# Optimization experiments

Hardware: AMD Instinct MI355X
Metric: run time of the kernel (lower is better)

## Reference

```python
import jax, jax.numpy as jnp
import numpy as np

B = 512      # batch
T = 16       # tokens per instruction
V = 1000     # vocab
E = 4        # num_experts
K = 1        # active experts per layer
NLAYERS = 3
TOPK_LOGIC = 32


def _conv(x, w, b, stride=2):
    # x: [B,Cin,H,W], w: [Cout,Cin,3,3] (OIHW), padding=1, stride=2
    y = jax.lax.conv_general_dilated(
        x, w, window_strides=(stride, stride), padding=((1, 1), (1, 1)),
        dimension_numbers=('NCHW', 'OIHW', 'NCHW'))
    return y + b[None, :, None, None]


def _gated_conv(x, w, b, gate):
    # w: [E,Cout,Cin,3,3], b: [E,Cout], gate: [B,E] 0/1 mask
    # Faithful to original: all experts computed densely, then masked.
    outs = jax.vmap(lambda wi, bi: _conv(x, wi, bi))(w, b)  # [E,B,Cout,H',W']
    return jnp.einsum('ebchw,be->bchw', outs, gate)


def _topk_mask(logits, k):
    # 0/1 mask with ones at the top-k positions along the last axis
    _, idx = jax.lax.top_k(logits, k)
    return jnp.sum(jax.nn.one_hot(idx, logits.shape[-1], dtype=logits.dtype), axis=-2)


def setup_inputs() -> dict:
    key = jax.random.key(0)
    ks = jax.random.split(key, 16)
    def rn(k, shape, s=0.05):
        return jax.random.normal(k, shape, jnp.float32) * s
    return dict(
        img=jax.random.normal(ks[0], (B, 12, 56, 56), jnp.float32),
        text=jax.random.randint(ks[1], (B, T), 0, V),
        prev_action=jax.random.randint(ks[2], (B,), 0, 7),
        emb_table=rn(ks[3], (V, 32), 1.0),
        r_w1=rn(ks[4], (32, 64)), r_b1=jnp.zeros((64,), jnp.float32),
        r_w2=rn(ks[5], (64, NLAYERS * E)), r_b2=jnp.zeros((NLAYERS * E,), jnp.float32),
        l_w1=rn(ks[6], (32, 64)), l_b1=jnp.zeros((64,), jnp.float32),
        l_w2=rn(ks[7], (64, 256)), l_b2=jnp.zeros((256,), jnp.float32),
        c1_w=rn(ks[8], (E, 32, 12, 3, 3)), c1_b=jnp.zeros((E, 32), jnp.float32),
        c2_w=rn(ks[9], (E, 64, 32, 3, 3)), c2_b=jnp.zeros((E, 64), jnp.float32),
        c3_w=rn(ks[10], (E, 128, 64, 3, 3)), c3_b=jnp.zeros((E, 128), jnp.float32),
        act_emb=rn(ks[11], (7, 16), 1.0),
        f_w=rn(ks[12], (6272 + 32 + 16, 256)), f_b=jnp.zeros((256,), jnp.float32),
        h_w=rn(ks[13], (256, 5)), h_b=jnp.zeros((5,), jnp.float32),
    )


def reference(img, text, prev_action, emb_table, r_w1, r_b1, r_w2, r_b2,
              l_w1, l_b1, l_w2, l_b2, c1_w, c1_b, c2_w, c2_b, c3_w, c3_b,
              act_emb, f_w, f_b, h_w, h_b):
    # EmbeddingBag(mode='mean') over token dim
    lang = jnp.mean(emb_table[text], axis=1)                      # [B,32]
    # Router: MLP -> [B,3,E] logits, top-k scatter -> 0/1 mask
    rlog = (jax.nn.relu(lang @ r_w1 + r_b1) @ r_w2 + r_b2).reshape(-1, NLAYERS, E)
    masks = _topk_mask(rlog, K)                                   # [B,3,E]
    x = jax.nn.relu(_gated_conv(img, c1_w, c1_b, masks[:, 0, :])) # [B,32,28,28]
    x = jax.nn.relu(_gated_conv(x, c2_w, c2_b, masks[:, 1, :]))   # [B,64,14,14]
    x = jax.nn.relu(_gated_conv(x, c3_w, c3_b, masks[:, 2, :]))   # [B,128,7,7]
    vis = x.reshape(x.shape[0], -1)                               # [B,6272]
    act = act_emb[prev_action]                                    # [B,16]
    fused = jnp.concatenate([vis, lang, act], axis=1)             # [B,6320]
    hidden = fused @ f_w + f_b                                    # [B,256]
    logic = jax.nn.relu(lang @ l_w1 + l_b1) @ l_w2 + l_b2         # [B,256]
    lmask = _topk_mask(logic, TOPK_LOGIC)                         # [B,256]
    out = jax.nn.relu(hidden * lmask)                             # dropout is identity in eval
    logits = out @ h_w + h_b                                      # [B,5]
    return logits, rlog
```

## Files before the change

### kernel.cpp

```cpp
#include <hip/hip_runtime.h>
#include <hip/hip_bf16.h>


typedef __bf16 bf16x8 __attribute__((ext_vector_type(8)));
typedef float f32x4 __attribute__((ext_vector_type(4)));

__device__ __forceinline__ unsigned short f2bf(float f) {
  union { float f; unsigned u; } v; v.f = f;
  unsigned r = v.u + 0x7FFFu + ((v.u >> 16) & 1u);
  return (unsigned short)(r >> 16);
}

__global__ __launch_bounds__(256) void router_kernel(
    const int* __restrict__ text, const float* __restrict__ emb,
    const float* __restrict__ r_w1, const float* __restrict__ r_b1,
    const float* __restrict__ r_w2, const float* __restrict__ r_b2,
    const float* __restrict__ l_w1, const float* __restrict__ l_b1,
    const float* __restrict__ l_w2, const float* __restrict__ l_b2,
    const float* __restrict__ act_emb, const int* __restrict__ pa,
    float* __restrict__ rlog_out, int* __restrict__ eidx, float* __restrict__ lmask,
    unsigned short* __restrict__ tailb) {
  int b = blockIdx.x;
  int t = threadIdx.x;
  __shared__ float lg[32];
  __shared__ float hr[64];
  __shared__ float hl[64];
  __shared__ float rl[12];
  __shared__ float lgc[256];

  if (t < 32) {
    const int* tb = text + b * 16;
    float s = 0.f;
#pragma unroll
    for (int tok = 0; tok < 16; ++tok) s += emb[tb[tok] * 32 + t];
    lg[t] = s * 0.0625f;
  }
  __syncthreads();

  if (t < 64) {
    float s1 = r_b1[t], s2 = l_b1[t];
    for (int k = 0; k < 32; ++k) {
      float lv = lg[k];
      s1 += lv * r_w1[k * 64 + t];
      s2 += lv * l_w1[k * 64 + t];
    }
    hr[t] = fmaxf(s1, 0.f);
    hl[t] = fmaxf(s2, 0.f);
  }
  if (t < 64) {
    float v = 0.f;
    if (t < 32) v = lg[t];
    else if (t < 48) v = act_emb[pa[b] * 16 + (t - 32)];
    tailb[b * 64 + t] = f2bf(v);
  }
  __syncthreads();

  if (t < 12) {
    float s = r_b2[t];
    for (int k = 0; k < 64; ++k) s += hr[k] * r_w2[k * 12 + t];
    rl[t] = s;
    rlog_out[b * 12 + t] = s;
  }
  {
    float s = l_b2[t];
    for (int k = 0; k < 64; ++k) s += hl[k] * l_w2[k * 256 + t];
    lgc[t] = s;
  }
  __syncthreads();

  if (t < 3) {
    int best = 0;
    float bv = rl[t * 4];
    for (int e = 1; e < 4; ++e) {
      float v = rl[t * 4 + e];
      if (v > bv) { bv = v; best = e; }
    }
    eidx[b * 3 + t] = best;
  }
  {
    float v = lgc[t];
    int cnt = 0;
    for (int k = 0; k < 256; ++k) {
      float u = lgc[k];
      cnt += (u > v) || (u == v && k < t);
    }
    lmask[b * 256 + t] = (cnt < 32) ? 1.f : 0.f;
  }
}

__global__ __launch_bounds__(256) void prep_kernel(
    const float* __restrict__ img,
    const float* __restrict__ c1_w, const float* __restrict__ c2_w,
    const float* __restrict__ c3_w, const float* __restrict__ fw,
    const int* __restrict__ eidx,
    unsigned short* __restrict__ x0b,
    unsigned short* __restrict__ wb1, unsigned short* __restrict__ wb2,
    unsigned short* __restrict__ wb3, unsigned short* __restrict__ fwT,
    int* __restrict__ cnt, int* __restrict__ perm) {
  __shared__ __align__(16) char shm[64 * 72 * 2];
  const int blk = blockIdx.x;
  const int tid = threadIdx.x;

  if (blk < 6272) {
    int idx = blk * 256 + tid;
    int s = idx / 3136;
    int p = idx - s * 3136;
    const float* ib = img + (size_t)s * 37632 + p;
    unsigned short v[16];
#pragma unroll
    for (int ci = 0; ci < 12; ++ci) v[ci] = f2bf(ib[ci * 3136]);
#pragma unroll
    for (int ci = 12; ci < 16; ++ci) v[ci] = 0;
    uint4* dst = (uint4*)(x0b + (size_t)idx * 16);
    dst[0] = *(const uint4*)&v[0];
    dst[1] = *(const uint4*)&v[8];
  } else if (blk < 7840) {
    int idx = (blk - 6272) * 256 + tid;
    if (idx < 24576) {
      int k = idx % 192, ec = idx / 192;
      float v = 0.f;
      if (k < 144) {
        int g = k >> 4, ci = k & 15;
        if (ci < 12) v = c1_w[ec * 108 + ci * 9 + g];
      }
      wb1[idx] = f2bf(v);
    } else if (idx < 106496) {
      int i2 = idx - 24576;
      int k = i2 % 320, ec = i2 / 320;
      float v = 0.f;
      if (k < 288) {
        int g = k >> 5, ci = k & 31;
        v = c2_w[ec * 288 + ci * 9 + g];
      }
      wb2[i2] = f2bf(v);
    } else {
      int i3 = idx - 106496;
      int k = i3 % 576, ec = i3 / 576;
      int g = k >> 6, ci = k & 63;
      wb3[i3] = f2bf(c3_w[ec * 576 + ci * 9 + g]);
    }
  } else if (blk < 8236) {
    unsigned short(*tl)[72] = (unsigned short(*)[72])shm;
    int fb = blk - 7840;
    int kblk = fb >> 2, nblk = fb & 3;
    int n0 = nblk * 64;
    int k0 = kblk * 64;
    int rl = tid >> 2;
    int c4 = (tid & 3) * 16;
    int srow;
    bool valid;
    if (kblk < 98) {
      int p = kblk >> 1;
      int c0 = (kblk & 1) * 64;
      srow = (c0 + rl) * 49 + p;
      valid = true;
    } else {
      srow = 6272 + rl;
      valid = (rl < 48);
    }
#pragma unroll
    for (int h = 0; h < 4; ++h) {
      float4 v = valid ? *(const float4*)&fw[(size_t)srow * 256 + n0 + c4 + h * 4]
                       : (float4){0.f, 0.f, 0.f, 0.f};
      tl[rl][c4 + h * 4 + 0] = f2bf(v.x);
      tl[rl][c4 + h * 4 + 1] = f2bf(v.y);
      tl[rl][c4 + h * 4 + 2] = f2bf(v.z);
      tl[rl][c4 + h * 4 + 3] = f2bf(v.w);
    }
    __syncthreads();
    int nloc = tid >> 2;
    int kc = (tid & 3) * 16;
    unsigned short vv[16];
#pragma unroll
    for (int i = 0; i < 16; ++i) vv[i] = tl[kc + i][nloc];
    unsigned short* dst = fwT + (size_t)(n0 + nloc) * 6336 + k0 + kc;
    *(uint4*)dst = *(const uint4*)&vv[0];
    *(uint4*)(dst + 8) = *(const uint4*)&vv[8];
  } else {
    int* el = (int*)shm;
    int* cc = el + 512;
    int l = blk - 8236;
    el[tid] = eidx[tid * 3 + l];
    el[tid + 256] = eidx[(tid + 256) * 3 + l];
    __syncthreads();
    if (tid < 4) {
      int c = 0;
      for (int b = 0; b < 512; ++b) c += (el[b] == tid);
      cc[tid] = c;
      cnt[l * 4 + tid] = c;
    }
    __syncthreads();
#pragma unroll
    for (int rep = 0; rep < 2; ++rep) {
      int b = tid + rep * 256;
      int e = el[b];
      int rank = 0;
      for (int bp = 0; bp < b; ++bp) rank += (el[bp] == e);
      int off = 0;
      for (int ee = 0; ee < e; ++ee) off += cc[ee];
      perm[l * 512 + off + rank] = b;
    }
  }
}

template<int CIN, int H, int OH, int KREAL, int KP, int COUT,
         int WGM, int WGN, int MF, int NF>
__global__ __launch_bounds__(256) void conv_mfma(
    const unsigned short* __restrict__ in, const unsigned short* __restrict__ wb,
    const float* __restrict__ bias, const int* __restrict__ cnt,
    const int* __restrict__ perm, unsigned short* __restrict__ out) {
  constexpr int PerS = OH * OH;
  constexpr int BM = WGM * MF * 16;
  constexpr int BN = WGN * NF * 16;
  constexpr int AJ = BM / 32;
  constexpr int KT = KP / 64;
  constexpr int W = H;
  constexpr int BCH = BN / 32;

  int bm = blockIdx.x;
  int e = 0, row0 = 0, rows = 0;
  bool found = false;
  {
    int acc = 0, ebase = 0;
#pragma unroll
    for (int ee = 0; ee < 4; ++ee) {
      int er = cnt[ee] * PerS;
      int te = (er + BM - 1) / BM;
      if (!found && bm < acc + te) {
        e = ee;
        row0 = ebase + (bm - acc) * BM;
        rows = er - (bm - acc) * BM;
        if (rows > BM) rows = BM;
        found = true;
      }
      acc += te;
      ebase += er;
    }
  }
  if (!found) return;

  __shared__ __align__(16) char lds[BM * 128 + BN * 128];
  char* ldsB = lds + BM * 128;
  const int tid = threadIdx.x;
  const int lane = tid & 63;
  const int wid = tid >> 6;
  const int wm0 = (wid / WGN) * (MF * 16);
  const int wn0 = (wid % WGN) * (NF * 16);
  const int c16 = tid & 7;

  int ihc[AJ], iwc[AJ], abase[AJ], adso[AJ];
#pragma unroll
  for (int j = 0; j < AJ; ++j) {
    int r = (tid >> 3) + 32 * j;
    int gr = row0 + r;
    const int MAXR = 512 * PerS - 1;
    if (gr > MAXR) gr = MAXR;
    int sord = gr / PerS;
    int p = gr - sord * PerS;
    int s = perm[sord];
    int oh = p / OH, ow = p - oh * OH;
    ihc[j] = oh * 2 - 1;
    iwc[j] = ow * 2 - 1;
    abase[j] = s * (H * W);
    adso[j] = r * 128 + ((c16 * 16) ^ ((r & 7) << 4));
  }
  const unsigned short* wbe = wb + (size_t)e * COUT * KP;
  int bgo[BCH], bdso[BCH];
#pragma unroll
  for (int c = 0; c < BCH; ++c) {
    int cc = tid + 256 * c;
    int n = cc >> 3, cb = cc & 7;
    bgo[c] = n * KP + cb * 8;
    bdso[c] = n * 128 + ((cb * 16) ^ ((n & 7) << 4));
  }
  int ardo[MF], arx[MF], brdo[NF], brx[NF];
#pragma unroll
  for (int mf = 0; mf < MF; ++mf) {
    int r = wm0 + mf * 16 + (lane & 15);
    ardo[mf] = r * 128;
    arx[mf] = (r & 7) << 4;
  }
#pragma unroll
  for (int nf = 0; nf < NF; ++nf) {
    int n = wn0 + nf * 16 + (lane & 15);
    brdo[nf] = n * 128;
    brx[nf] = (n & 7) << 4;
  }

  auto loadA = [&](int kt, int j) -> uint4 {
    uint4 z; z.x = z.y = z.z = z.w = 0u;
    int kbase = kt * 64 + c16 * 8;
    if (kbase >= KREAL) return z;
    int g = kbase / CIN;
    int ci0 = kbase - g * CIN;
    int kh = g / 3, kw = g - (g / 3) * 3;
    int ih = ihc[j] + kh, iw = iwc[j] + kw;
    if ((unsigned)ih >= (unsigned)H || (unsigned)iw >= (unsigned)W) return z;
    const unsigned short* p = in + ((size_t)(abase[j] + ih * W + iw) * CIN + ci0);
    return *(const uint4*)p;
  };

  uint4 rA[AJ], rB[BCH];
#pragma unroll
  for (int j = 0; j < AJ; ++j) rA[j] = loadA(0, j);
#pragma unroll
  for (int c = 0; c < BCH; ++c) rB[c] = *(const uint4*)(wbe + bgo[c]);

  f32x4 acc[MF][NF];
#pragma unroll
  for (int mf = 0; mf < MF; ++mf)
#pragma unroll
    for (int nf = 0; nf < NF; ++nf) acc[mf][nf] = (f32x4){0.f, 0.f, 0.f, 0.f};

  for (int kt = 0; kt < KT; ++kt) {
    __syncthreads();
#pragma unroll
    for (int j = 0; j < AJ; ++j) *(uint4*)(lds + adso[j]) = rA[j];
#pragma unroll
    for (int c = 0; c < BCH; ++c) *(uint4*)(ldsB + bdso[c]) = rB[c];
    __syncthreads();
    if (kt + 1 < KT) {
#pragma unroll
      for (int j = 0; j < AJ; ++j) rA[j] = loadA(kt + 1, j);
#pragma unroll
      for (int c = 0; c < BCH; ++c) rB[c] = *(const uint4*)(wbe + bgo[c] + (kt + 1) * 64);
    }
#pragma unroll
    for (int ks = 0; ks < 2; ++ks) {
      int cb = ks * 64 + ((lane >> 4) << 4);
      bf16x8 af[MF], bfv[NF];
#pragma unroll
      for (int mf = 0; mf < MF; ++mf)
        af[mf] = __builtin_bit_cast(bf16x8, *(const uint4*)(lds + ardo[mf] + (cb ^ arx[mf])));
#pragma unroll
      for (int nf = 0; nf < NF; ++nf)
        bfv[nf] = __builtin_bit_cast(bf16x8, *(const uint4*)(ldsB + brdo[nf] + (cb ^ brx[nf])));
#pragma unroll
      for (int mf = 0; mf < MF; ++mf)
#pragma unroll
        for (int nf = 0; nf < NF; ++nf)
          acc[mf][nf] = __builtin_amdgcn_mfma_f32_16x16x32_bf16(af[mf], bfv[nf], acc[mf][nf], 0, 0, 0);
    }
  }

  const int col = lane & 15;
  const int rg = (lane >> 4) * 4;
#pragma unroll
  for (int mf = 0; mf < MF; ++mf) {
#pragma unroll
    for (int r = 0; r < 4; ++r) {
      int m = wm0 + mf * 16 + rg + r;
      if (m < rows) {
        int gr = row0 + m;
        int sord = gr / PerS;
        int p = gr - sord * PerS;
        int s = perm[sord];
        size_t ob = ((size_t)s * PerS + p) * COUT;
#pragma unroll
        for (int nf = 0; nf < NF; ++nf) {
          int co = wn0 + nf * 16 + col;
          float v = acc[mf][nf][r] + bias[e * COUT + co];
          out[ob + co] = f2bf(fmaxf(v, 0.f));
        }
      }
    }
  }
}

__global__ __launch_bounds__(256) void fgemm_kernel(
    const unsigned short* __restrict__ x3, const unsigned short* __restrict__ tail,
    const unsigned short* __restrict__ fwT, float* __restrict__ partial) {
  constexpr int MF = 2, NF = 2;
  const int row0 = blockIdx.x * 64;
  const int nc0 = blockIdx.y * 64;
  const int kz = blockIdx.z * 704;
  __shared__ __align__(16) char lds[64 * 128 + 64 * 128];
  char* ldsB = lds + 64 * 128;
  const int tid = threadIdx.x;
  const int lane = tid & 63;
  const int wid = tid >> 6;
  const int wm0 = (wid >> 1) * 32;
  const int wn0 = (wid & 1) * 32;
  const int c16 = tid & 7;
  int arow[2], adso[2];
#pragma unroll
  for (int j = 0; j < 2; ++j) {
    int r = (tid >> 3) + 32 * j;
    arow[j] = row0 + r;
    adso[j] = r * 128 + ((c16 * 16) ^ ((r & 7) << 4));
  }
  int bgo[2], bdso[2];
#pragma unroll
  for (int c = 0; c < 2; ++c) {
    int cc = tid + 256 * c;
    int n = cc >> 3, cb = cc & 7;
    bgo[c] = (nc0 + n) * 6336 + kz + cb * 8;
    bdso[c] = n * 128 + ((cb * 16) ^ ((n & 7) << 4));
  }
  int ardo[MF], arx[MF], brdo[NF], brx[NF];
#pragma unroll
  for (int mf = 0; mf < MF; ++mf) {
    int r = wm0 + mf * 16 + (lane & 15);
    ardo[mf] = r * 128; arx[mf] = (r & 7) << 4;
  }
#pragma unroll
  for (int nf = 0; nf < NF; ++nf) {
    int n = wn0 + nf * 16 + (lane & 15);
    brdo[nf] = n * 128; brx[nf] = (n & 7) << 4;
  }
  auto loadA = [&](int kt, int j) -> uint4 {
    int k = kz + kt * 64 + c16 * 8;
    const unsigned short* p;
    if (k < 6272) p = x3 + (size_t)arow[j] * 6272 + k;
    else p = tail + arow[j] * 64 + (k - 6272);
    return *(const uint4*)p;
  };
  uint4 rA[2], rB[2];
#pragma unroll
  for (int j = 0; j < 2; ++j) rA[j] = loadA(0, j);
#pragma unroll
  for (int c = 0; c < 2; ++c) rB[c] = *(const uint4*)(fwT + bgo[c]);
  f32x4 acc[MF][NF];
#pragma unroll
  for (int mf = 0; mf < MF; ++mf)
#pragma unroll
    for (int nf = 0; nf < NF; ++nf) acc[mf][nf] = (f32x4){0.f, 0.f, 0.f, 0.f};

  for (int kt = 0; kt < 11; ++kt) {
    __syncthreads();
#pragma unroll
    for (int j = 0; j < 2; ++j) *(uint4*)(lds + adso[j]) = rA[j];
#pragma unroll
    for (int c = 0; c < 2; ++c) *(uint4*)(ldsB + bdso[c]) = rB[c];
    __syncthreads();
    if (kt + 1 < 11) {
#pragma unroll
      for (int j = 0; j < 2; ++j) rA[j] = loadA(kt + 1, j);
#pragma unroll
      for (int c = 0; c < 2; ++c) rB[c] = *(const uint4*)(fwT + bgo[c] + (kt + 1) * 64);
    }
#pragma unroll
    for (int ks = 0; ks < 2; ++ks) {
      int cb = ks * 64 + ((lane >> 4) << 4);
      bf16x8 af[MF], bfv[NF];
#pragma unroll
      for (int mf = 0; mf < MF; ++mf)
        af[mf] = __builtin_bit_cast(bf16x8, *(const uint4*)(lds + ardo[mf] + (cb ^ arx[mf])));
#pragma unroll
      for (int nf = 0; nf < NF; ++nf)
        bfv[nf] = __builtin_bit_cast(bf16x8, *(const uint4*)(ldsB + brdo[nf] + (cb ^ brx[nf])));
#pragma unroll
      for (int mf = 0; mf < MF; ++mf)
#pragma unroll
        for (int nf = 0; nf < NF; ++nf)
          acc[mf][nf] = __builtin_amdgcn_mfma_f32_16x16x32_bf16(af[mf], bfv[nf], acc[mf][nf], 0, 0, 0);
    }
  }
  const int col = lane & 15;
  const int rg = (lane >> 4) * 4;
  float* pz = partial + (size_t)blockIdx.z * 131072;
#pragma unroll
  for (int mf = 0; mf < MF; ++mf)
#pragma unroll
    for (int r = 0; r < 4; ++r) {
      int m = wm0 + mf * 16 + rg + r;
      int grow = row0 + m;
#pragma unroll
      for (int nf = 0; nf < NF; ++nf) {
        int n = nc0 + wn0 + nf * 16 + col;
        pz[grow * 256 + n] = acc[mf][nf][r];
      }
    }
}

__global__ __launch_bounds__(256) void reduce_head(const float* __restrict__ part,
                                                   const float* __restrict__ f_b,
                                                   const float* __restrict__ lmask,
                                                   const float* __restrict__ h_w,
                                                   const float* __restrict__ h_b,
                                                   float* __restrict__ logits) {
  int b = blockIdx.x, t = threadIdx.x;
  float s = f_b[t];
#pragma unroll
  for (int z = 0; z < 9; ++z) s += part[z * 131072 + b * 256 + t];
  __shared__ float o[256];
  o[t] = (lmask[b * 256 + t] != 0.f) ? fmaxf(s, 0.f) : 0.f;
  __syncthreads();
  if (t < 5) {
    float v = h_b[t];
    for (int n = 0; n < 256; ++n) v += o[n] * h_w[n * 5 + t];
    logits[b * 5 + t] = v;
  }
}

extern "C" void kernel_launch(void* const* d_in, const int* in_sizes, int n_in,
                              void* d_out, int out_size, void* d_ws, size_t ws_size,
                              hipStream_t stream) {
  (void)in_sizes; (void)n_in; (void)out_size; (void)ws_size;
  const float* img       = (const float*)d_in[0];
  const int*   text      = (const int*)d_in[1];
  const int*   pa        = (const int*)d_in[2];
  const float* emb_table = (const float*)d_in[3];
  const float* r_w1 = (const float*)d_in[4];
  const float* r_b1 = (const float*)d_in[5];
  const float* r_w2 = (const float*)d_in[6];
  const float* r_b2 = (const float*)d_in[7];
  const float* l_w1 = (const float*)d_in[8];
  const float* l_b1 = (const float*)d_in[9];
  const float* l_w2 = (const float*)d_in[10];
  const float* l_b2 = (const float*)d_in[11];
  const float* c1_w = (const float*)d_in[12];
  const float* c1_b = (const float*)d_in[13];
  const float* c2_w = (const float*)d_in[14];
  const float* c2_b = (const float*)d_in[15];
  const float* c3_w = (const float*)d_in[16];
  const float* c3_b = (const float*)d_in[17];
  const float* act_emb = (const float*)d_in[18];
  const float* f_w = (const float*)d_in[19];
  const float* f_b = (const float*)d_in[20];
  const float* h_w = (const float*)d_in[21];
  const float* h_b = (const float*)d_in[22];

  float* outf   = (float*)d_out;
  float* logits = outf;
  float* rlog   = outf + 2560;

  char* cur = (char*)d_ws;
  auto alloc = [&](size_t bytes) { char* r = cur; cur += (bytes + 255) & ~(size_t)255; return r; };
  float* lmask   = (float*)alloc(131072 * 4);
  int* eidx      = (int*)alloc(1536 * 4);
  int* cnt       = (int*)alloc(12 * 4);
  int* perm      = (int*)alloc(1536 * 4);
  unsigned short* wb1  = (unsigned short*)alloc((size_t)24576 * 2);
  unsigned short* wb2  = (unsigned short*)alloc((size_t)81920 * 2);
  unsigned short* wb3  = (unsigned short*)alloc((size_t)294912 * 2);
  unsigned short* fwT  = (unsigned short*)alloc((size_t)1622016 * 2);
  unsigned short* tailb= (unsigned short*)alloc((size_t)32768 * 2);
  unsigned short* x1b  = (unsigned short*)alloc((size_t)12845056 * 2);
  unsigned short* x0b  = (unsigned short*)alloc((size_t)25690112 * 2);
  unsigned short* x2b  = x0b;
  unsigned short* x3b  = x0b + 6422528;
  float* partial       = (float*)(x0b + 6422528 + 3211264);

  router_kernel<<<512, 256, 0, stream>>>(text, emb_table, r_w1, r_b1, r_w2, r_b2,
                                         l_w1, l_b1, l_w2, l_b2, act_emb, pa,
                                         rlog, eidx, lmask, tailb);
  prep_kernel<<<8239, 256, 0, stream>>>(img, c1_w, c2_w, c3_w, f_w, eidx,
                                        x0b, wb1, wb2, wb3, fwT, cnt, perm);

  conv_mfma<16, 56, 28, 144, 192, 32, 4, 1, 2, 2>
      <<<3139, 256, 0, stream>>>(x0b, wb1, c1_b, cnt + 0, perm + 0, x1b);
  conv_mfma<32, 28, 14, 288, 320, 64, 2, 2, 4, 2>
      <<<787, 256, 0, stream>>>(x1b, wb2, c2_b, cnt + 4, perm + 512, x2b);
  conv_mfma<64, 14, 7, 576, 576, 128, 1, 4, 4, 2>
      <<<395, 256, 0, stream>>>(x2b, wb3, c3_b, cnt + 8, perm + 1024, x3b);

  fgemm_kernel<<<dim3(8, 4, 9), 256, 0, stream>>>(x3b, tailb, fwT, partial);
  reduce_head<<<512, 256, 0, stream>>>(partial, f_b, lmask, h_w, h_b, logits);
}
```

Baseline: 160.2 us.

## Fuse router into prep kernel, split bucketing out, vectorize image conversion

The router work moves into the prep kernel as its first 512 blocks, so it runs alongside the weight and image conversion. The expert bucketing, which needs the router output, moves into its own small kernel launched after prep. This keeps the launch count the same but lets router work overlap with prep. The image NCHW→NHWC bf16 conversion now handles 4 pixels per thread with float4 loads, which cuts the prep grid from 8239 to 4044 blocks at the cost of more registers per thread.

```diff
diff --git a/kernel.cpp b/kernel.cpp
--- a/kernel.cpp
+++ b/kernel.cpp
@@ -11,111 +11,94 @@
   return (unsigned short)(r >> 16);
 }
 
-__global__ __launch_bounds__(256) void router_kernel(
+__global__ __launch_bounds__(256) void prep_kernel(
+    const float* __restrict__ img,
     const int* __restrict__ text, const float* __restrict__ emb,
     const float* __restrict__ r_w1, const float* __restrict__ r_b1,
     const float* __restrict__ r_w2, const float* __restrict__ r_b2,
     const float* __restrict__ l_w1, const float* __restrict__ l_b1,
     const float* __restrict__ l_w2, const float* __restrict__ l_b2,
     const float* __restrict__ act_emb, const int* __restrict__ pa,
-    float* __restrict__ rlog_out, int* __restrict__ eidx, float* __restrict__ lmask,
-    unsigned short* __restrict__ tailb) {
-  int b = blockIdx.x;
-  int t = threadIdx.x;
-  __shared__ float lg[32];
-  __shared__ float hr[64];
-  __shared__ float hl[64];
-  __shared__ float rl[12];
-  __shared__ float lgc[256];
-
-  if (t < 32) {
-    const int* tb = text + b * 16;
-    float s = 0.f;
-#pragma unroll
-    for (int tok = 0; tok < 16; ++tok) s += emb[tb[tok] * 32 + t];
-    lg[t] = s * 0.0625f;
-  }
-  __syncthreads();
-
-  if (t < 64) {
-    float s1 = r_b1[t], s2 = l_b1[t];
-    for (int k = 0; k < 32; ++k) {
-      float lv = lg[k];
-      s1 += lv * r_w1[k * 64 + t];
-      s2 += lv * l_w1[k * 64 + t];
-    }
-    hr[t] = fmaxf(s1, 0.f);
-    hl[t] = fmaxf(s2, 0.f);
-  }
-  if (t < 64) {
-    float v = 0.f;
-    if (t < 32) v = lg[t];
-    else if (t < 48) v = act_emb[pa[b] * 16 + (t - 32)];
-    tailb[b * 64 + t] = f2bf(v);
-  }
-  __syncthreads();
-
-  if (t < 12) {
-    float s = r_b2[t];
-    for (int k = 0; k < 64; ++k) s += hr[k] * r_w2[k * 12 + t];
-    rl[t] = s;
-    rlog_out[b * 12 + t] = s;
-  }
-  {
-    float s = l_b2[t];
-    for (int k = 0; k < 64; ++k) s += hl[k] * l_w2[k * 256 + t];
-    lgc[t] = s;
-  }
-  __syncthreads();
-
-  if (t < 3) {
-    int best = 0;
-    float bv = rl[t * 4];
-    for (int e = 1; e < 4; ++e) {
-      float v = rl[t * 4 + e];
-      if (v > bv) { bv = v; best = e; }
-    }
-    eidx[b * 3 + t] = best;
-  }
-  {
-    float v = lgc[t];
-    int cnt = 0;
-    for (int k = 0; k < 256; ++k) {
-      float u = lgc[k];
-      cnt += (u > v) || (u == v && k < t);
-    }
-    lmask[b * 256 + t] = (cnt < 32) ? 1.f : 0.f;
-  }
-}
-
-__global__ __launch_bounds__(256) void prep_kernel(
-    const float* __restrict__ img,
     const float* __restrict__ c1_w, const float* __restrict__ c2_w,
     const float* __restrict__ c3_w, const float* __restrict__ fw,
-    const int* __restrict__ eidx,
+    float* __restrict__ rlog_out, int* __restrict__ eidx, float* __restrict__ lmask,
+    unsigned short* __restrict__ tailb,
     unsigned short* __restrict__ x0b,
     unsigned short* __restrict__ wb1, unsigned short* __restrict__ wb2,
-    unsigned short* __restrict__ wb3, unsigned short* __restrict__ fwT,
-    int* __restrict__ cnt, int* __restrict__ perm) {
+    unsigned short* __restrict__ wb3, unsigned short* __restrict__ fwT) {
   __shared__ __align__(16) char shm[64 * 72 * 2];
   const int blk = blockIdx.x;
   const int tid = threadIdx.x;
 
-  if (blk < 6272) {
-    int idx = blk * 256 + tid;
-    int s = idx / 3136;
-    int p = idx - s * 3136;
-    const float* ib = img + (size_t)s * 37632 + p;
-    unsigned short v[16];
-#pragma unroll
-    for (int ci = 0; ci < 12; ++ci) v[ci] = f2bf(ib[ci * 3136]);
-#pragma unroll
-    for (int ci = 12; ci < 16; ++ci) v[ci] = 0;
-    uint4* dst = (uint4*)(x0b + (size_t)idx * 16);
-    dst[0] = *(const uint4*)&v[0];
-    dst[1] = *(const uint4*)&v[8];
-  } else if (blk < 7840) {
-    int idx = (blk - 6272) * 256 + tid;
+  if (blk < 512) {
+    int b = blk;
+    int t = tid;
+    __shared__ float lg[32];
+    __shared__ float hr[64];
+    __shared__ float hl[64];
+    __shared__ float rl[12];
+    __shared__ float lgc[256];
+
+    if (t < 32) {
+      const int* tb = text + b * 16;
+      float s = 0.f;
+#pragma unroll
+      for (int tok = 0; tok < 16; ++tok) s += emb[tb[tok] * 32 + t];
+      lg[t] = s * 0.0625f;
+    }
+    __syncthreads();
+
+    if (t < 64) {
+      float s1 = r_b1[t], s2 = l_b1[t];
+      for (int k = 0; k < 32; ++k) {
+        float lv = lg[k];
+        s1 += lv * r_w1[k * 64 + t];
+        s2 += lv * l_w1[k * 64 + t];
+      }
+      hr[t] = fmaxf(s1, 0.f);
+      hl[t] = fmaxf(s2, 0.f);
+    }
+    if (t < 64) {
+      float v = 0.f;
+      if (t < 32) v = lg[t];
+      else if (t < 48) v = act_emb[pa[b] * 16 + (t - 32)];
+      tailb[b * 64 + t] = f2bf(v);
+    }
+    __syncthreads();
+
+    if (t < 12) {
+      float s = r_b2[t];
+      for (int k = 0; k < 64; ++k) s += hr[k] * r_w2[k * 12 + t];
+      rl[t] = s;
+      rlog_out[b * 12 + t] = s;
+    }
+    {
+      float s = l_b2[t];
+      for (int k = 0; k < 64; ++k) s += hl[k] * l_w2[k * 256 + t];
+      lgc[t] = s;
+    }
+    __syncthreads();
+
+    if (t < 3) {
+      int best = 0;
+      float bv = rl[t * 4];
+      for (int e = 1; e < 4; ++e) {
+        float v = rl[t * 4 + e];
+        if (v > bv) { bv = v; best = e; }
+      }
+      eidx[b * 3 + t] = best;
+    }
+    {
+      float v = lgc[t];
+      int cnt = 0;
+      for (int k = 0; k < 256; ++k) {
+        float u = lgc[k];
+        cnt += (u > v) || (u == v && k < t);
+      }
+      lmask[b * 256 + t] = (cnt < 32) ? 1.f : 0.f;
+    }
+  } else if (blk < 2080) {
+    int idx = (blk - 512) * 256 + tid;
     if (idx < 24576) {
       int k = idx % 192, ec = idx / 192;
       float v = 0.f;
@@ -139,9 +122,9 @@
       int g = k >> 6, ci = k & 63;
       wb3[i3] = f2bf(c3_w[ec * 576 + ci * 9 + g]);
     }
-  } else if (blk < 8236) {
+  } else if (blk < 2476) {
     unsigned short(*tl)[72] = (unsigned short(*)[72])shm;
-    int fb = blk - 7840;
+    int fb = blk - 2080;
     int kblk = fb >> 2, nblk = fb & 3;
     int n0 = nblk * 64;
     int k0 = kblk * 64;
@@ -177,29 +160,57 @@
     *(uint4*)dst = *(const uint4*)&vv[0];
     *(uint4*)(dst + 8) = *(const uint4*)&vv[8];
   } else {
-    int* el = (int*)shm;
-    int* cc = el + 512;
-    int l = blk - 8236;
-    el[tid] = eidx[tid * 3 + l];
-    el[tid + 256] = eidx[(tid + 256) * 3 + l];
-    __syncthreads();
-    if (tid < 4) {
-      int c = 0;
-      for (int b = 0; b < 512; ++b) c += (el[b] == tid);
-      cc[tid] = c;
-      cnt[l * 4 + tid] = c;
-    }
-    __syncthreads();
-#pragma unroll
-    for (int rep = 0; rep < 2; ++rep) {
-      int b = tid + rep * 256;
-      int e = el[b];
-      int rank = 0;
-      for (int bp = 0; bp < b; ++bp) rank += (el[bp] == e);
-      int off = 0;
-      for (int ee = 0; ee < e; ++ee) off += cc[ee];
-      perm[l * 512 + off + rank] = b;
-    }
+    int idx4 = (blk - 2476) * 256 + tid;
+    int s = idx4 / 784;
+    int q = idx4 - s * 784;
+    const float* ib = img + (size_t)s * 37632 + q * 4;
+    float4 v[12];
+#pragma unroll
+    for (int ci = 0; ci < 12; ++ci) v[ci] = *(const float4*)&ib[ci * 3136];
+    unsigned short o16[64];
+#pragma unroll
+    for (int j = 0; j < 4; ++j) {
+      o16[j * 16 + 0]  = f2bf(j == 0 ? v[0].x : j == 1 ? v[0].y : j == 2 ? v[0].z : v[0].w);
+#pragma unroll
+      for (int ci = 1; ci < 12; ++ci) {
+        float fv = (j == 0) ? v[ci].x : (j == 1) ? v[ci].y : (j == 2) ? v[ci].z : v[ci].w;
+        o16[j * 16 + ci] = f2bf(fv);
+      }
+#pragma unroll
+      for (int ci = 12; ci < 16; ++ci) o16[j * 16 + ci] = 0;
+    }
+    uint4* dst = (uint4*)(x0b + (size_t)idx4 * 64);
+#pragma unroll
+    for (int h = 0; h < 8; ++h) dst[h] = *(const uint4*)&o16[h * 8];
+  }
+}
+
+__global__ __launch_bounds__(256) void bucket_kernel(const int* __restrict__ eidx,
+                                                     int* __restrict__ cnt,
+                                                     int* __restrict__ perm) {
+  int l = blockIdx.x;
+  __shared__ int el[512];
+  __shared__ int cc[4];
+  int t = threadIdx.x;
+  el[t] = eidx[t * 3 + l];
+  el[t + 256] = eidx[(t + 256) * 3 + l];
+  __syncthreads();
+  if (t < 4) {
+    int c = 0;
+    for (int b = 0; b < 512; ++b) c += (el[b] == t);
+    cc[t] = c;
+    cnt[l * 4 + t] = c;
+  }
+  __syncthreads();
+#pragma unroll
+  for (int rep = 0; rep < 2; ++rep) {
+    int b = t + rep * 256;
+    int e = el[b];
+    int rank = 0;
+    for (int bp = 0; bp < b; ++bp) rank += (el[bp] == e);
+    int off = 0;
+    for (int ee = 0; ee < e; ++ee) off += cc[ee];
+    perm[l * 512 + off + rank] = b;
   }
 }
 
@@ -542,11 +553,14 @@
   unsigned short* x3b  = x0b + 6422528;
   float* partial       = (float*)(x0b + 6422528 + 3211264);
 
-  router_kernel<<<512, 256, 0, stream>>>(text, emb_table, r_w1, r_b1, r_w2, r_b2,
-                                         l_w1, l_b1, l_w2, l_b2, act_emb, pa,
-                                         rlog, eidx, lmask, tailb);
-  prep_kernel<<<8239, 256, 0, stream>>>(img, c1_w, c2_w, c3_w, f_w, eidx,
-                                        x0b, wb1, wb2, wb3, fwT, cnt, perm);
+  prep_kernel<<<4044, 256, 0, stream>>>(img, text, emb_table,
+                                        r_w1, r_b1, r_w2, r_b2,
+                                        l_w1, l_b1, l_w2, l_b2,
+                                        act_emb, pa,
+                                        c1_w, c2_w, c3_w, f_w,
+                                        rlog, eidx, lmask, tailb,
+                                        x0b, wb1, wb2, wb3, fwT);
+  bucket_kernel<<<3, 256, 0, stream>>>(eidx, cnt, perm);
 
   conv_mfma<16, 56, 28, 144, 192, 32, 4, 1, 2, 2>
       <<<3139, 256, 0, stream>>>(x0b, wb1, c1_b, cnt + 0, perm + 0, x1b);
```

Result: faster. 156.3 us (-2.4%).
